# Performance work log

Measured on AMD Instinct MI355X. Metric: run time of the kernel, lower is better.

Reference implementation:

```python
import jax, jax.numpy as jnp
import numpy as np

N = 10000      # nodes of this type
T = 160000     # total metapath instances (ragged rows)
D = 256        # input_dim
P = 256        # pre_embed_dim
H = 512        # mlp_settings['layer_list'][0]
S = 64         # select_dim


def setup_inputs() -> dict:
    key = jax.random.key(0)
    ks = jax.random.split(key, 16)
    def w(k, shape):
        return jax.random.normal(k, shape, jnp.float32) / np.sqrt(shape[0]).astype(np.float32)
    return {
        "feat_A": jax.random.normal(ks[0], (N, D), jnp.float32),
        "feat_AP": jax.random.normal(ks[1], (T, D), jnp.float32),
        "feat_APA": jax.random.normal(ks[2], (T, 2 * D), jnp.float32),
        "seg_AP": jnp.sort(jax.random.randint(ks[3], (T,), 0, N, jnp.int32)),
        "seg_APA": jnp.sort(jax.random.randint(ks[4], (T,), 0, N, jnp.int32)),
        "type_weight": w(ks[5], (D, P)),
        "W_enc_AP": w(ks[6], (D, H)),   "b_enc_AP": jnp.zeros((H,), jnp.float32),
        "W_dec_AP": w(ks[7], (H, P)),   "b_dec_AP": jnp.zeros((P,), jnp.float32),
        "W_enc_APA": w(ks[8], (2 * D, H)), "b_enc_APA": jnp.zeros((H,), jnp.float32),
        "W_dec_APA": w(ks[9], (H, P)),  "b_dec_APA": jnp.zeros((P,), jnp.float32),
        "W_attn1": w(ks[10], (2 * P, 2 * P)),
        "W_attn2": w(ks[11], (2 * P, 1)),
        "W_cls": w(ks[12], (P, S)), "b_cls": jnp.zeros((S,), jnp.float32),
    }


def reference(feat_A, feat_AP, feat_APA, seg_AP, seg_APA, type_weight,
              W_enc_AP, b_enc_AP, W_dec_AP, b_dec_AP,
              W_enc_APA, b_enc_APA, W_dec_APA, b_dec_APA,
              W_attn1, W_attn2, W_cls, b_cls):
    # center node embedding (metapath of length 1): feat @ type_weight
    center = feat_A @ type_weight                                  # [N, P]

    def metapath_path(feat, seg, We, be, Wd, bd):
        # per-metapath MLP encode (Linear+ReLU) / decode (Linear)
        h = jax.nn.relu(feat @ We + be)                            # [T, H]
        dec = h @ Wd + bd                                          # [T, P]
        # ragged split + per-node sum aggregation; empty segments -> zeros
        return jax.ops.segment_sum(dec, seg, num_segments=N,
                                   indices_are_sorted=True)        # [N, P]

    inj_AP = metapath_path(feat_AP, seg_AP, W_enc_AP, b_enc_AP, W_dec_AP, b_dec_AP)
    inj_APA = metapath_path(feat_APA, seg_APA, W_enc_APA, b_enc_APA, W_dec_APA, b_dec_APA)

    def attn_score(inj):
        # attn = Tanh -> Linear(2P,2P,no bias) -> Linear(2P,1,no bias) -> LeakyReLU(0.1), then mean
        x = jnp.tanh(jnp.concatenate([center, inj], axis=1))       # [N, 2P]
        s = (x @ W_attn1) @ W_attn2                                # [N, 1]
        return jax.nn.leaky_relu(s, 0.1).mean()

    # index 0 corresponds to the length-1 metapath (never scored; fixed to 0)
    scores = jnp.stack([jnp.zeros((), jnp.float32), attn_score(inj_AP), attn_score(inj_APA)])
    wts = jax.nn.softmax(scores)                                   # [3]

    inj_AP = inj_AP * wts[1]
    inj_APA = inj_APA * wts[2]
    embed = (inj_AP + inj_APA) * 0.5                               # stack(...,dim=2).mean(dim=2)
    pre_embed = jax.nn.log_softmax((center + embed) @ W_cls + b_cls, axis=1)  # [N, S]
    return pre_embed, inj_AP, inj_APA
```

## Files before the change

kernel.cpp:

```cpp
#include <hip/hip_runtime.h>
#include <stdint.h>

typedef __bf16 bf16x8 __attribute__((ext_vector_type(8)));
typedef __bf16 bf16x4 __attribute__((ext_vector_type(4)));
typedef float  f32x4  __attribute__((ext_vector_type(4)));

#define N_NODES 10000
#define T_ROWS  160000
#define HDIM    512
#define PDIM    256
#define NCTILES 157
#define PACK_BLKS 177
#define ZERO_BLKS 256

__device__ __forceinline__ f32x4 mfma16(bf16x8 a, bf16x8 b, f32x4 c) {
    return __builtin_amdgcn_mfma_f32_16x16x32_bf16(a, b, c, 0, 0, 0);
}

__device__ __forceinline__ void pack_one(const float* __restrict__ W,
                                         __bf16* __restrict__ out,
                                         int K, int Nc, int ltid) {
    int lane = ltid & 63;
    int t = ltid >> 6;
    int KT = K >> 5;
    int kt = t % KT, nt = t / KT;
    int col = (nt << 4) + (lane & 15);
    int krow = (kt << 5) + ((lane >> 4) << 3);
    __bf16* dst = out + ((size_t)ltid << 3);
#pragma unroll
    for (int e = 0; e < 8; ++e)
        dst[e] = (__bf16)W[(size_t)(krow + e) * Nc + col];
}

__global__ void prep_kernel(
    const float* __restrict__ tw,    __bf16* __restrict__ twP,
    const float* __restrict__ WeAP,  __bf16* __restrict__ WeAPp,
    const float* __restrict__ WdAP,  __bf16* __restrict__ WdAPp,
    const float* __restrict__ WeAPA, __bf16* __restrict__ WeAPAp,
    const float* __restrict__ WdAPA, __bf16* __restrict__ WdAPAp,
    const float* __restrict__ W1, const float* __restrict__ W2,
    float* __restrict__ vbuf,
    float* __restrict__ injAP ,
    float* __restrict__ sacc)
{
    if (blockIdx.x >= PACK_BLKS) {
        int ztid = (blockIdx.x - PACK_BLKS) * 512 + threadIdx.x;
        f32x4 z = {0.f, 0.f, 0.f, 0.f};
        f32x4* dst = (f32x4*)injAP;
        for (int i = ztid; i < 2 * N_NODES * 64; i += ZERO_BLKS * 512)
            dst[i] = z;
        if (blockIdx.x == PACK_BLKS && threadIdx.x < 2) sacc[threadIdx.x] = 0.f;
        return;
    }
    int tid = blockIdx.x * 512 + threadIdx.x;
    if      (tid <  8192) pack_one(tw,    twP,    256, 256, tid);
    else if (tid < 24576) pack_one(WeAP,  WeAPp,  256, 512, tid - 8192);
    else if (tid < 40960) pack_one(WdAP,  WdAPp,  512, 256, tid - 24576);
    else if (tid < 73728) pack_one(WeAPA, WeAPAp, 512, 512, tid - 40960);
    else if (tid < 90112) pack_one(WdAPA, WdAPAp, 512, 256, tid - 73728);
    else if (tid < 90624) {
        int k = tid - 90112;
        float s = 0.f;
        for (int j = 0; j < 512; ++j) s += W1[k * 512 + j] * W2[j];
        vbuf[k] = s;
    }
}

template<int DIN>
__device__ __forceinline__ void path_body(
    const float* __restrict__ X,
    const __bf16* __restrict__ WeP, const float* __restrict__ be,
    const __bf16* __restrict__ WdP, const float* __restrict__ bd,
    const int* __restrict__ seg,
    float* __restrict__ inj,
    int tile, __bf16* buf, int* segs)
{
    constexpr int LDX = DIN + 8;
    constexpr int LDH = HDIM + 8;
    constexpr int LDP = 260;
    constexpr int KT1 = DIN / 32;
    const int tid = threadIdx.x;
    const int row0 = tile * 64;
    if (tid < 64) segs[tid] = seg[row0 + tid];

#pragma unroll 4
    for (int i = tid; i < 64 * (DIN / 4); i += 512) {
        int r = i / (DIN / 4), c4 = i % (DIN / 4);
        float4 f = ((const float4*)X)[(size_t)(row0 + r) * (DIN / 4) + c4];
        bf16x4 h;
        h[0] = (__bf16)f.x; h[1] = (__bf16)f.y; h[2] = (__bf16)f.z; h[3] = (__bf16)f.w;
        *(bf16x4*)&buf[r * LDX + c4 * 4] = h;
    }
    __syncthreads();

    const int wave = tid >> 6, lane = tid & 63;
    const int lr = lane & 15, lg = lane >> 4;

    f32x4 acc1[4][4] = {};
    {
        const __bf16* w1 = WeP + ((size_t)(wave * 4) * KT1) * 512 + lane * 8;
        bf16x8 bX[4], bY[4], a[4];
#pragma unroll
        for (int ct = 0; ct < 4; ++ct) bX[ct] = *(const bf16x8*)&w1[(size_t)(ct * KT1) * 512];
        for (int kt = 0; kt < KT1; kt += 2) {
#pragma unroll
            for (int ct = 0; ct < 4; ++ct)
                bY[ct] = *(const bf16x8*)&w1[(size_t)(ct * KT1 + kt + 1) * 512];
            int ko = kt * 32 + lg * 8;
#pragma unroll
            for (int rt = 0; rt < 4; ++rt)
                a[rt] = *(const bf16x8*)&buf[(rt * 16 + lr) * LDX + ko];
            __builtin_amdgcn_s_setprio(1);
#pragma unroll
            for (int ct = 0; ct < 4; ++ct)
#pragma unroll
                for (int rt = 0; rt < 4; ++rt)
                    acc1[rt][ct] = mfma16(a[rt], bX[ct], acc1[rt][ct]);
            __builtin_amdgcn_s_setprio(0);
            int kn = (kt + 2 < KT1) ? kt + 2 : 0;
#pragma unroll
            for (int ct = 0; ct < 4; ++ct)
                bX[ct] = *(const bf16x8*)&w1[(size_t)(ct * KT1 + kn) * 512];
            ko = (kt + 1) * 32 + lg * 8;
#pragma unroll
            for (int rt = 0; rt < 4; ++rt)
                a[rt] = *(const bf16x8*)&buf[(rt * 16 + lr) * LDX + ko];
            __builtin_amdgcn_s_setprio(1);
#pragma unroll
            for (int ct = 0; ct < 4; ++ct)
#pragma unroll
                for (int rt = 0; rt < 4; ++rt)
                    acc1[rt][ct] = mfma16(a[rt], bY[ct], acc1[rt][ct]);
            __builtin_amdgcn_s_setprio(0);
        }
    }
    __syncthreads();

#pragma unroll
    for (int ct = 0; ct < 4; ++ct) {
        int col = wave * 64 + ct * 16 + lr;
        float bias = be[col];
#pragma unroll
        for (int rt = 0; rt < 4; ++rt) {
            int rbase = rt * 16 + lg * 4;
#pragma unroll
            for (int j = 0; j < 4; ++j) {
                float vl = acc1[rt][ct][j] + bias;
                buf[(rbase + j) * LDH + col] = (__bf16)(vl > 0.f ? vl : 0.f);
            }
        }
    }
    __syncthreads();

    f32x4 acc2[4][2] = {};
    {
        const __bf16* w2 = WdP + ((size_t)(wave * 2) * 16) * 512 + lane * 8;
        bf16x8 bX2[2], bY2[2], aX[4], aY[4];
#pragma unroll
        for (int ct = 0; ct < 2; ++ct) bX2[ct] = *(const bf16x8*)&w2[(size_t)(ct * 16) * 512];
#pragma unroll
        for (int rt = 0; rt < 4; ++rt)
            aX[rt] = *(const bf16x8*)&buf[(rt * 16 + lr) * LDH + lg * 8];
        for (int kt = 0; kt < 16; kt += 2) {
#pragma unroll
            for (int ct = 0; ct < 2; ++ct)
                bY2[ct] = *(const bf16x8*)&w2[(size_t)(ct * 16 + kt + 1) * 512];
            int ko = (kt + 1) * 32 + lg * 8;
#pragma unroll
            for (int rt = 0; rt < 4; ++rt)
                aY[rt] = *(const bf16x8*)&buf[(rt * 16 + lr) * LDH + ko];
            __builtin_amdgcn_s_setprio(1);
#pragma unroll
            for (int ct = 0; ct < 2; ++ct)
#pragma unroll
                for (int rt = 0; rt < 4; ++rt)
                    acc2[rt][ct] = mfma16(aX[rt], bX2[ct], acc2[rt][ct]);
            __builtin_amdgcn_s_setprio(0);
            int kn = (kt + 2 < 16) ? kt + 2 : 0;
#pragma unroll
            for (int ct = 0; ct < 2; ++ct)
                bX2[ct] = *(const bf16x8*)&w2[(size_t)(ct * 16 + kn) * 512];
            ko = kn * 32 + lg * 8;
#pragma unroll
            for (int rt = 0; rt < 4; ++rt)
                aX[rt] = *(const bf16x8*)&buf[(rt * 16 + lr) * LDH + ko];
            __builtin_amdgcn_s_setprio(1);
#pragma unroll
            for (int ct = 0; ct < 2; ++ct)
#pragma unroll
                for (int rt = 0; rt < 4; ++rt)
                    acc2[rt][ct] = mfma16(aY[rt], bY2[ct], acc2[rt][ct]);
            __builtin_amdgcn_s_setprio(0);
        }
    }
    __syncthreads();

    float* decs = (float*)buf;
#pragma unroll
    for (int ct = 0; ct < 2; ++ct) {
        int col = wave * 32 + ct * 16 + lr;
        float bias = bd[col];
#pragma unroll
        for (int rt = 0; rt < 4; ++rt) {
            int rbase = rt * 16 + lg * 4;
#pragma unroll
            for (int j = 0; j < 4; ++j)
                decs[(rbase + j) * LDP + col] = acc2[rt][ct][j] + bias;
        }
    }

    {
        const int c  = wave * 32 + (lane & 31);
        const int rs = (lane >> 5) * 32;
        float run = decs[rs * LDP + c];
        int cur = segs[rs];
        int runstart = rs;
#pragma unroll
        for (int r = rs + 1; r < rs + 32; ++r) {
            int s = segs[r];
            float v = decs[r * LDP + c];
            if (s == cur) run += v;
            else {
                if (runstart != rs) inj[(size_t)cur * PDIM + c] = run;
                else atomicAdd(&inj[(size_t)cur * PDIM + c], run);
                cur = s; run = v; runstart = r;
            }
        }
        atomicAdd(&inj[(size_t)cur * PDIM + c], run);
    }
}

__device__ __forceinline__ void center_body(
    const float* __restrict__ feat, const __bf16* __restrict__ twP,
    float* __restrict__ center, int tile, __bf16* xs)
{
    constexpr int LDX = 264;
    const int tid = threadIdx.x;
    const int row0 = tile * 64;
#pragma unroll 4
    for (int i = tid; i < 64 * 64; i += 512) {
        int r = i / 64, c4 = i % 64;
        int row = row0 + r;
        float4 f = {0.f, 0.f, 0.f, 0.f};
        if (row < N_NODES) f = ((const float4*)feat)[(size_t)row * 64 + c4];
        bf16x4 h;
        h[0] = (__bf16)f.x; h[1] = (__bf16)f.y; h[2] = (__bf16)f.z; h[3] = (__bf16)f.w;
        *(bf16x4*)&xs[r * LDX + c4 * 4] = h;
    }
    __syncthreads();

    const int wave = tid >> 6, lane = tid & 63;
    const int lr = lane & 15, lg = lane >> 4;
    f32x4 acc[4][2] = {};
    const __bf16* w = twP + ((size_t)(wave * 2) * 8) * 512 + lane * 8;
    for (int kt = 0; kt < 8; ++kt) {
        int ko = kt * 32 + lg * 8;
        bf16x8 a[4];
#pragma unroll
        for (int rt = 0; rt < 4; ++rt)
            a[rt] = *(const bf16x8*)&xs[(rt * 16 + lr) * LDX + ko];
#pragma unroll
        for (int ct = 0; ct < 2; ++ct) {
            bf16x8 b = *(const bf16x8*)&w[(size_t)(ct * 8 + kt) * 512];
#pragma unroll
            for (int rt = 0; rt < 4; ++rt)
                acc[rt][ct] = mfma16(a[rt], b, acc[rt][ct]);
        }
    }
#pragma unroll
    for (int ct = 0; ct < 2; ++ct) {
        int col = wave * 32 + ct * 16 + lr;
#pragma unroll
        for (int rt = 0; rt < 4; ++rt) {
            int rbase = rt * 16 + lg * 4;
#pragma unroll
            for (int j = 0; j < 4; ++j) {
                int row = row0 + rbase + j;
                if (row < N_NODES) center[(size_t)row * 256 + col] = acc[rt][ct][j];
            }
        }
    }
}

__global__ __launch_bounds__(512, 4) void paths_kernel(
    const float* __restrict__ featAP,  const float* __restrict__ featAPA,
    const __bf16* __restrict__ WeAPp,  const float* __restrict__ beAP,
    const __bf16* __restrict__ WdAPp,  const float* __restrict__ bdAP,
    const __bf16* __restrict__ WeAPAp, const float* __restrict__ beAPA,
    const __bf16* __restrict__ WdAPAp, const float* __restrict__ bdAPA,
    const int* __restrict__ segAP, const int* __restrict__ segAPA,
    float* __restrict__ injAP, float* __restrict__ injAPA,
    const float* __restrict__ featA, const __bf16* __restrict__ twP,
    float* __restrict__ center)
{
    __shared__ __bf16 buf[64 * (HDIM + 8)];
    __shared__ int segs[64];
    int bid = blockIdx.x;
    if (bid < NCTILES) {
        center_body(featA, twP, center, bid, buf);
        return;
    }
    int p = bid - NCTILES;
    int tile = p >> 1;
    if (p & 1)
        path_body<512>(featAPA, WeAPAp, beAPA, WdAPAp, bdAPA, segAPA, injAPA,
                       tile, buf, segs);
    else
        path_body<256>(featAP, WeAPp, beAP, WdAPp, bdAP, segAP, injAP,
                       tile, buf, segs);
}

__global__ __launch_bounds__(256, 4) void score2_kernel(
    const float* __restrict__ center, const float* __restrict__ injAP,
    const float* __restrict__ injAPA, const float* __restrict__ v,
    float* __restrict__ sacc)
{
    const int w = threadIdx.x >> 6, lane = threadIdx.x & 63;
    float l1 = 0.f, l2 = 0.f;
    for (int row = blockIdx.x * 4 + w; row < N_NODES; row += gridDim.x * 4) {
        float x1 = 0.f, x2 = 0.f;
#pragma unroll
        for (int k = 0; k < 4; ++k) {
            int c = lane + k * 64;
            size_t off = (size_t)row * 256 + c;
            float tc = tanhf(center[off]) * v[c];
            float vi = v[256 + c];
            x1 += tc + tanhf(injAP[off]) * vi;
            x2 += tc + tanhf(injAPA[off]) * vi;
        }
#pragma unroll
        for (int o = 32; o > 0; o >>= 1) {
            x1 += __shfl_xor(x1, o);
            x2 += __shfl_xor(x2, o);
        }
        if (lane == 0) {
            l1 += (x1 > 0.f) ? x1 : 0.1f * x1;
            l2 += (x2 > 0.f) ? x2 : 0.1f * x2;
        }
    }
    if (lane == 0) {
        atomicAdd(&sacc[0], l1);
        atomicAdd(&sacc[1], l2);
    }
}

__global__ __launch_bounds__(256, 4) void final_kernel(
    const float* __restrict__ center, const float* __restrict__ injAP,
    const float* __restrict__ injAPA, const float* __restrict__ sacc,
    const float* __restrict__ Wcls, const float* __restrict__ bcls,
    float* __restrict__ out0, float* __restrict__ out1, float* __restrict__ out2)
{
    __shared__ float zs[4][256];
    float s1 = sacc[0] * (1.f / N_NODES), s2 = sacc[1] * (1.f / N_NODES);
    float m0 = fmaxf(0.f, fmaxf(s1, s2));
    float e0 = expf(0.f - m0), e1 = expf(s1 - m0), e2 = expf(s2 - m0);
    float inv = 1.f / (e0 + e1 + e2);
    const float w1 = e1 * inv, w2 = e2 * inv;

    const int row0 = blockIdx.x * 4;
    for (int idx = threadIdx.x; idx < 1024; idx += 256) {
        int r = idx >> 8, c = idx & 255;
        size_t off = (size_t)(row0 + r) * 256 + c;
        float a = injAP[off] * w1, b = injAPA[off] * w2;
        out1[off] = a; out2[off] = b;
        zs[r][c] = center[off] + 0.5f * (a + b);
    }
    __syncthreads();
    const int g = threadIdx.x >> 6, j = threadIdx.x & 63;
    float p0 = bcls[j], p1 = 0.f, p2 = 0.f, p3 = 0.f;
#pragma unroll 4
    for (int k = 0; k < 256; k += 4) {
        p0 += zs[g][k + 0] * Wcls[(k + 0) * 64 + j];
        p1 += zs[g][k + 1] * Wcls[(k + 1) * 64 + j];
        p2 += zs[g][k + 2] * Wcls[(k + 2) * 64 + j];
        p3 += zs[g][k + 3] * Wcls[(k + 3) * 64 + j];
    }
    float logit = (p0 + p1) + (p2 + p3);
    float m = logit;
#pragma unroll
    for (int o = 32; o > 0; o >>= 1) m = fmaxf(m, __shfl_xor(m, o));
    float e = expf(logit - m);
    float se = e;
#pragma unroll
    for (int o = 32; o > 0; o >>= 1) se += __shfl_xor(se, o);
    out0[(size_t)(row0 + g) * 64 + j] = (logit - m) - logf(se);
}

extern "C" void kernel_launch(void* const* d_in, const int* in_sizes, int n_in,
                              void* d_out, int out_size, void* d_ws, size_t ws_size,
                              hipStream_t stream)
{
    const float* feat_A   = (const float*)d_in[0];
    const float* feat_AP  = (const float*)d_in[1];
    const float* feat_APA = (const float*)d_in[2];
    const int*   seg_AP   = (const int*)d_in[3];
    const int*   seg_APA  = (const int*)d_in[4];
    const float* type_w   = (const float*)d_in[5];
    const float* We_AP    = (const float*)d_in[6];
    const float* be_AP    = (const float*)d_in[7];
    const float* Wd_AP    = (const float*)d_in[8];
    const float* bd_AP    = (const float*)d_in[9];
    const float* We_APA   = (const float*)d_in[10];
    const float* be_APA   = (const float*)d_in[11];
    const float* Wd_APA   = (const float*)d_in[12];
    const float* bd_APA   = (const float*)d_in[13];
    const float* W_attn1  = (const float*)d_in[14];
    const float* W_attn2  = (const float*)d_in[15];
    const float* W_cls    = (const float*)d_in[16];
    const float* b_cls    = (const float*)d_in[17];

    char* ws = (char*)d_ws;
    size_t o = 0;
    auto alloc = [&](size_t bytes) { char* p = ws + o; o += (bytes + 255) & ~size_t(255); return p; };
    float* center = (float*)alloc((size_t)N_NODES * 256 * 4);
    float* injAP  = (float*)alloc((size_t)N_NODES * 256 * 4);
    float* injAPA = (float*)alloc((size_t)N_NODES * 256 * 4);
    float* vbuf   = (float*)alloc(512 * 4);
    float* sacc   = (float*)alloc(256);
    __bf16* twP    = (__bf16*)alloc(256 * 256 * 2);
    __bf16* WeAPp  = (__bf16*)alloc(256 * 512 * 2);
    __bf16* WdAPp  = (__bf16*)alloc(512 * 256 * 2);
    __bf16* WeAPAp = (__bf16*)alloc(512 * 512 * 2);
    __bf16* WdAPAp = (__bf16*)alloc(512 * 256 * 2);

    prep_kernel<<<PACK_BLKS + ZERO_BLKS, 512, 0, stream>>>(
        type_w, twP, We_AP, WeAPp, Wd_AP, WdAPp,
        We_APA, WeAPAp, Wd_APA, WdAPAp,
        W_attn1, W_attn2, vbuf, injAP, sacc);
    paths_kernel<<<NCTILES + 2 * (T_ROWS / 64), 512, 0, stream>>>(
        feat_AP, feat_APA, WeAPp, be_AP, WdAPp, bd_AP,
        WeAPAp, be_APA, WdAPAp, bd_APA, seg_AP, seg_APA, injAP, injAPA,
        feat_A, twP, center);
    score2_kernel<<<256, 256, 0, stream>>>(center, injAP, injAPA, vbuf, sacc);

    float* out0 = (float*)d_out;
    float* out1 = out0 + (size_t)N_NODES * 64;
    float* out2 = out1 + (size_t)N_NODES * 256;
    final_kernel<<<N_NODES / 4, 256, 0, stream>>>(center, injAP, injAPA, sacc,
                                                  W_cls, b_cls, out0, out1, out2);
}
```

Before: 421.9 us.

## Double path-tile rows to 128 with 1024-thread blocks sharing weight columns

The path MLP tile grows from 64 to 128 rows per block, with 16 waves split into two row halves that share column slices of the encoder and decoder weights. Each weight fragment is now read from global/L2 for twice as many rows, so total weight traffic drops. The cost is double the LDS per block (about 133KB) and 1024-thread blocks, which limits occupancy to one block per CU. The center tiles keep 64 rows and leave the extra waves idle.

```diff
diff --git a/kernel.cpp b/kernel.cpp
--- a/kernel.cpp
+++ b/kernel.cpp
@@ -9,6 +9,8 @@
 #define T_ROWS  160000
 #define HDIM    512
 #define PDIM    256
+#define BM      128
+#define NPT     1250
 #define NCTILES 157
 #define PACK_BLKS 177
 #define ZERO_BLKS 256
@@ -80,11 +82,11 @@
     constexpr int LDP = 260;
     constexpr int KT1 = DIN / 32;
     const int tid = threadIdx.x;
-    const int row0 = tile * 64;
-    if (tid < 64) segs[tid] = seg[row0 + tid];
+    const int row0 = tile * BM;
+    if (tid < BM) segs[tid] = seg[row0 + tid];
 
 #pragma unroll 4
-    for (int i = tid; i < 64 * (DIN / 4); i += 512) {
+    for (int i = tid; i < BM * (DIN / 4); i += 1024) {
         int r = i / (DIN / 4), c4 = i % (DIN / 4);
         float4 f = ((const float4*)X)[(size_t)(row0 + r) * (DIN / 4) + c4];
         bf16x4 h;
@@ -94,11 +96,13 @@
     __syncthreads();
 
     const int wave = tid >> 6, lane = tid & 63;
+    const int rh = (wave & 1) * 64;
+    const int cs = wave >> 1;
     const int lr = lane & 15, lg = lane >> 4;
 
     f32x4 acc1[4][4] = {};
     {
-        const __bf16* w1 = WeP + ((size_t)(wave * 4) * KT1) * 512 + lane * 8;
+        const __bf16* w1 = WeP + ((size_t)(cs * 4) * KT1) * 512 + lane * 8;
         bf16x8 bX[4], bY[4], a[4];
 #pragma unroll
         for (int ct = 0; ct < 4; ++ct) bX[ct] = *(const bf16x8*)&w1[(size_t)(ct * KT1) * 512];
@@ -109,7 +113,7 @@
             int ko = kt * 32 + lg * 8;
 #pragma unroll
             for (int rt = 0; rt < 4; ++rt)
-                a[rt] = *(const bf16x8*)&buf[(rt * 16 + lr) * LDX + ko];
+                a[rt] = *(const bf16x8*)&buf[(rh + rt * 16 + lr) * LDX + ko];
             __builtin_amdgcn_s_setprio(1);
 #pragma unroll
             for (int ct = 0; ct < 4; ++ct)
@@ -124,7 +128,7 @@
             ko = (kt + 1) * 32 + lg * 8;
 #pragma unroll
             for (int rt = 0; rt < 4; ++rt)
-                a[rt] = *(const bf16x8*)&buf[(rt * 16 + lr) * LDX + ko];
+                a[rt] = *(const bf16x8*)&buf[(rh + rt * 16 + lr) * LDX + ko];
             __builtin_amdgcn_s_setprio(1);
 #pragma unroll
             for (int ct = 0; ct < 4; ++ct)
@@ -138,11 +142,11 @@
 
 #pragma unroll
     for (int ct = 0; ct < 4; ++ct) {
-        int col = wave * 64 + ct * 16 + lr;
+        int col = cs * 64 + ct * 16 + lr;
         float bias = be[col];
 #pragma unroll
         for (int rt = 0; rt < 4; ++rt) {
-            int rbase = rt * 16 + lg * 4;
+            int rbase = rh + rt * 16 + lg * 4;
 #pragma unroll
             for (int j = 0; j < 4; ++j) {
                 float vl = acc1[rt][ct][j] + bias;
@@ -154,13 +158,13 @@
 
     f32x4 acc2[4][2] = {};
     {
-        const __bf16* w2 = WdP + ((size_t)(wave * 2) * 16) * 512 + lane * 8;
+        const __bf16* w2 = WdP + ((size_t)(cs * 2) * 16) * 512 + lane * 8;
         bf16x8 bX2[2], bY2[2], aX[4], aY[4];
 #pragma unroll
         for (int ct = 0; ct < 2; ++ct) bX2[ct] = *(const bf16x8*)&w2[(size_t)(ct * 16) * 512];
 #pragma unroll
         for (int rt = 0; rt < 4; ++rt)
-            aX[rt] = *(const bf16x8*)&buf[(rt * 16 + lr) * LDH + lg * 8];
+            aX[rt] = *(const bf16x8*)&buf[(rh + rt * 16 + lr) * LDH + lg * 8];
         for (int kt = 0; kt < 16; kt += 2) {
 #pragma unroll
             for (int ct = 0; ct < 2; ++ct)
@@ -168,7 +172,7 @@
             int ko = (kt + 1) * 32 + lg * 8;
 #pragma unroll
             for (int rt = 0; rt < 4; ++rt)
-                aY[rt] = *(const bf16x8*)&buf[(rt * 16 + lr) * LDH + ko];
+                aY[rt] = *(const bf16x8*)&buf[(rh + rt * 16 + lr) * LDH + ko];
             __builtin_amdgcn_s_setprio(1);
 #pragma unroll
             for (int ct = 0; ct < 2; ++ct)
@@ -183,7 +187,7 @@
             ko = kn * 32 + lg * 8;
 #pragma unroll
             for (int rt = 0; rt < 4; ++rt)
-                aX[rt] = *(const bf16x8*)&buf[(rt * 16 + lr) * LDH + ko];
+                aX[rt] = *(const bf16x8*)&buf[(rh + rt * 16 + lr) * LDH + ko];
             __builtin_amdgcn_s_setprio(1);
 #pragma unroll
             for (int ct = 0; ct < 2; ++ct)
@@ -198,11 +202,11 @@
     float* decs = (float*)buf;
 #pragma unroll
     for (int ct = 0; ct < 2; ++ct) {
-        int col = wave * 32 + ct * 16 + lr;
+        int col = cs * 32 + ct * 16 + lr;
         float bias = bd[col];
 #pragma unroll
         for (int rt = 0; rt < 4; ++rt) {
-            int rbase = rt * 16 + lg * 4;
+            int rbase = rh + rt * 16 + lg * 4;
 #pragma unroll
             for (int j = 0; j < 4; ++j)
                 decs[(rbase + j) * LDP + col] = acc2[rt][ct][j] + bias;
@@ -210,8 +214,8 @@
     }
 
     {
-        const int c  = wave * 32 + (lane & 31);
-        const int rs = (lane >> 5) * 32;
+        const int c  = cs * 32 + (lane & 31);
+        const int rs = rh + (lane >> 5) * 32;
         float run = decs[rs * LDP + c];
         int cur = segs[rs];
         int runstart = rs;
@@ -238,7 +242,7 @@
     const int tid = threadIdx.x;
     const int row0 = tile * 64;
 #pragma unroll 4
-    for (int i = tid; i < 64 * 64; i += 512) {
+    for (int i = tid; i < 64 * 64; i += 1024) {
         int r = i / 64, c4 = i % 64;
         int row = row0 + r;
         float4 f = {0.f, 0.f, 0.f, 0.f};
@@ -250,6 +254,7 @@
     __syncthreads();
 
     const int wave = tid >> 6, lane = tid & 63;
+    if (wave >= 8) return;
     const int lr = lane & 15, lg = lane >> 4;
     f32x4 acc[4][2] = {};
     const __bf16* w = twP + ((size_t)(wave * 2) * 8) * 512 + lane * 8;
@@ -282,7 +287,7 @@
     }
 }
 
-__global__ __launch_bounds__(512, 4) void paths_kernel(
+__global__ __launch_bounds__(1024, 4) void paths_kernel(
     const float* __restrict__ featAP,  const float* __restrict__ featAPA,
     const __bf16* __restrict__ WeAPp,  const float* __restrict__ beAP,
     const __bf16* __restrict__ WdAPp,  const float* __restrict__ bdAP,
@@ -293,8 +298,8 @@
     const float* __restrict__ featA, const __bf16* __restrict__ twP,
     float* __restrict__ center)
 {
-    __shared__ __bf16 buf[64 * (HDIM + 8)];
-    __shared__ int segs[64];
+    __shared__ __bf16 buf[BM * (HDIM + 8)];
+    __shared__ int segs[BM];
     int bid = blockIdx.x;
     if (bid < NCTILES) {
         center_body(featA, twP, center, bid, buf);
@@ -427,7 +432,7 @@
         type_w, twP, We_AP, WeAPp, Wd_AP, WdAPp,
         We_APA, WeAPAp, Wd_APA, WdAPAp,
         W_attn1, W_attn2, vbuf, injAP, sacc);
-    paths_kernel<<<NCTILES + 2 * (T_ROWS / 64), 512, 0, stream>>>(
+    paths_kernel<<<NCTILES + 2 * NPT, 1024, 0, stream>>>(
         feat_AP, feat_APA, WeAPp, be_AP, WdAPp, bd_AP,
         WeAPAp, be_APA, WdAPAp, bd_APA, seg_AP, seg_APA, injAP, injAPA,
         feat_A, twP, center);
```

Result: slower. 454.8 us (+7.8%).
